# Kernel tuning notes

Measured on AMD Instinct MI355X. Metric: run time of the kernel, lower is better.

Reference implementation:

```python
import jax, jax.numpy as jnp
import numpy as np

N, M, E = 50000, 50000, 1600000
D_IN, HID, OUT = 128, 128, 128


def setup_inputs() -> dict:
    key = jax.random.key(0)
    ks = jax.random.split(key, 8)
    query = jax.random.normal(ks[0], (N, D_IN), jnp.float32)
    memory = jax.random.normal(ks[1], (M, D_IN), jnp.float32)
    adj_vals = jnp.ones((E,), jnp.float32)  # tf.sparse adjacency values (typically 1.0)
    Wq = jax.random.normal(ks[2], (D_IN, HID), jnp.float32) * 0.05
    bq = jnp.zeros((HID,), jnp.float32)
    Wk = jax.random.normal(ks[3], (D_IN, HID), jnp.float32) * 0.05
    bk = jnp.zeros((HID,), jnp.float32)
    Wv = jax.random.normal(ks[4], (D_IN, OUT), jnp.float32) * 0.05
    bv = jnp.zeros((OUT,), jnp.float32)
    rows = jnp.sort(jax.random.randint(ks[5], (E,), 0, N, jnp.int32))
    cols = jax.random.randint(ks[6], (E,), 0, M, jnp.int32)
    return {"query": query, "memory": memory, "adj_vals": adj_vals,
            "Wq": Wq, "bq": bq, "Wk": Wk, "bk": bk, "Wv": Wv, "bv": bv,
            "rows": rows, "cols": cols}


def reference(query, memory, adj_vals, Wq, bq, Wk, bk, Wv, bv, rows, cols):
    n = query.shape[0]
    hid = Wq.shape[1]
    # Dense projections with gelu (tfa.activations.gelu default approximate=True)
    q = jax.nn.gelu(query @ Wq + bq, approximate=True)   # [n, hid]
    k = jax.nn.gelu(memory @ Wk + bk, approximate=True)  # [m, hid]
    v = jax.nn.gelu(memory @ Wv + bv, approximate=True)  # [m, out]
    # Edge-level scores = (q_i . k_j) / sqrt(hid) * adj_val  (== coef * adj_matrix)
    scores = jnp.sum(q[rows] * k[cols], axis=-1)          # [E]
    scores = scores * (adj_vals / jnp.sqrt(jnp.float32(hid)))
    # Sparse softmax over nonzero entries of each row (tf.sparse.softmax)
    row_max = jax.ops.segment_max(scores, rows, num_segments=n, indices_are_sorted=True)
    row_max = jnp.where(jnp.isfinite(row_max), row_max, 0.0)  # rows with no edges
    e = jnp.exp(scores - row_max[rows])
    denom = jax.ops.segment_sum(e, rows, num_segments=n, indices_are_sorted=True)
    w = e / denom[rows]                                   # [E]
    # Sparse-dense matmul: out_i = sum_j w_ij * v_j
    out = jax.ops.segment_sum(w[:, None] * v[cols], rows, num_segments=n, indices_are_sorted=True)
    return out
```

## Files before the change

kernel.cpp:

```cpp
#include <hip/hip_runtime.h>
#include <hip/hip_bf16.h>
#include <math.h>

typedef _Float16 f16x4 __attribute__((ext_vector_type(4)));
typedef _Float16 f16x8 __attribute__((ext_vector_type(8)));
typedef float f32x4 __attribute__((ext_vector_type(4)));

#define DIM 128
#define LDST 136

__global__ __launch_bounds__(256) void prep_w_kernel(
    const float* __restrict__ Wq, const float* __restrict__ Wk,
    const float* __restrict__ Wv, _Float16* __restrict__ Wt)
{
    const float* W = (blockIdx.y == 0) ? Wq : (blockIdx.y == 1) ? Wk : Wv;
    _Float16* dst = Wt + (size_t)blockIdx.y * DIM * DIM;
    int idx = blockIdx.x * 256 + threadIdx.x;
    int k = idx >> 7;
    int n = idx & 127;
    dst[n * DIM + k] = (_Float16)W[idx];
}

__global__ __launch_bounds__(256) void row_ptr_kernel(
    const int* __restrict__ rows, int* __restrict__ row_ptr, int n, int e)
{
    int r = blockIdx.x * 256 + threadIdx.x;
    if (r > n) return;
    if (r == n) { row_ptr[n] = e; return; }
    int lo = 0, hi = e;
    while (lo < hi) {
        int mid = (lo + hi) >> 1;
        if (rows[mid] < r) lo = mid + 1; else hi = mid;
    }
    row_ptr[r] = lo;
}

__global__ __launch_bounds__(256, 2) void proj_gemm_kernel(
    const float* __restrict__ query, const float* __restrict__ memory,
    const _Float16* __restrict__ Wt,
    const float* __restrict__ bq, const float* __restrict__ bk,
    const float* __restrict__ bv,
    _Float16* __restrict__ qf, _Float16* __restrict__ kv, int n, int m)
{
    __shared__ _Float16 xs[128 * LDST];

    int which = blockIdx.y;
    const float* X    = (which == 0) ? query : memory;
    const _Float16* Wm = Wt + (size_t)which * DIM * DIM;
    const float* bias = (which == 0) ? bq : (which == 1) ? bk : bv;
    int R             = (which == 0) ? n : m;
    _Float16* Ybase   = (which == 0) ? qf : (which == 2) ? kv + DIM : kv;
    size_t Ystride    = (which == 0) ? DIM : 2 * DIM;

    int tid = threadIdx.x;
    int rowblock = blockIdx.x * 128;
    if (rowblock >= R) return;

    for (int it = 0; it < 16; ++it) {
        int flat = it * 256 + tid;
        int r  = flat >> 5;
        int c4 = (flat & 31) * 4;
        int gr = rowblock + r;
        if (gr >= R) gr = R - 1;
        float4 x = *(const float4*)(X + (size_t)gr * DIM + c4);
        f16x4 w4;
        w4[0] = (_Float16)x.x; w4[1] = (_Float16)x.y;
        w4[2] = (_Float16)x.z; w4[3] = (_Float16)x.w;
        *(f16x4*)(&xs[r * LDST + c4]) = w4;
    }
    __syncthreads();

    int wave = tid >> 6;
    int lane = tid & 63;
    int quad = lane >> 4;
    int l16  = lane & 15;
    int wrow = wave * 32;

    f16x8 afrag[2][4];
    for (int rt = 0; rt < 2; ++rt)
        for (int ks = 0; ks < 4; ++ks)
            afrag[rt][ks] = *(const f16x8*)(&xs[(wrow + rt * 16 + l16) * LDST + quad * 8 + ks * 32]);

    f32x4 acc[8][2];
    for (int ct = 0; ct < 8; ++ct) { acc[ct][0] = {0,0,0,0}; acc[ct][1] = {0,0,0,0}; }
    for (int ct = 0; ct < 8; ++ct) {
        const _Float16* wp = Wm + (size_t)(ct * 16 + l16) * DIM + quad * 8;
        for (int ks = 0; ks < 4; ++ks) {
            f16x8 b = *(const f16x8*)(wp + ks * 32);
            acc[ct][0] = __builtin_amdgcn_mfma_f32_16x16x32_f16(afrag[0][ks], b, acc[ct][0], 0, 0, 0);
            acc[ct][1] = __builtin_amdgcn_mfma_f32_16x16x32_f16(afrag[1][ks], b, acc[ct][1], 0, 0, 0);
        }
    }

    __syncthreads();
    for (int ct = 0; ct < 8; ++ct) {
        float bval = bias[ct * 16 + l16];
        for (int rt = 0; rt < 2; ++rt) {
            for (int reg = 0; reg < 4; ++reg) {
                float x = acc[ct][rt][reg] + bval;
                float t  = 0.7978845608028654f * (x + 0.044715f * x * x * x);
                float th = 1.0f - 2.0f / (__expf(2.0f * t) + 1.0f);
                float g  = 0.5f * x * (1.0f + th);
                xs[(wrow + rt * 16 + quad * 4 + reg) * LDST + ct * 16 + l16] = (_Float16)g;
            }
        }
    }
    __syncthreads();

    for (int it = 0; it < 8; ++it) {
        int flat = it * 256 + tid;
        int r  = flat >> 4;
        int c8 = (flat & 15) * 8;
        int gr = rowblock + r;
        if (gr < R) {
            f16x8 vv = *(const f16x8*)(&xs[r * LDST + c8]);
            *(f16x8*)(Ybase + (size_t)gr * Ystride + c8) = vv;
        }
    }
}

__global__ __launch_bounds__(256) void edge_attn_kernel(
    const _Float16* __restrict__ qf, const _Float16* __restrict__ kv,
    const float* __restrict__ adj_vals, const int* __restrict__ cols,
    const int* __restrict__ row_ptr, float* __restrict__ out, int n)
{
    int row = blockIdx.x * 4 + (threadIdx.x >> 6);
    if (row >= n) return;
    int lane    = threadIdx.x & 63;
    int quarter = lane >> 4;
    int l16     = lane & 15;

    int start = row_ptr[row];
    int end   = row_ptr[row + 1];

    float qv[8];
    {
        f16x8 qb = *(const f16x8*)(qf + (size_t)row * DIM + l16 * 8);
        for (int j = 0; j < 8; ++j) qv[j] = (float)qb[j];
    }

    float m_q = -1e30f, s_q = 0.0f;
    float acc[8];
    for (int j = 0; j < 8; ++j) acc[j] = 0.0f;

    const float scale = 0.08838834764831845f;

    for (int g = start; g < end; g += 8) {
        int eA = g + quarter;
        int eB = g + 4 + quarter;
        bool vA = eA < end;
        bool vB = eB < end;
        int   cA = vA ? cols[eA]     : 0;
        int   cB = vB ? cols[eB]     : 0;
        float aA = vA ? adj_vals[eA] : 0.0f;
        float aB = vB ? adj_vals[eB] : 0.0f;
        const _Float16* pA = kv + (size_t)cA * 256 + l16 * 8;
        const _Float16* pB = kv + (size_t)cB * 256 + l16 * 8;
        f16x8 kA = *(const f16x8*)pA;
        f16x8 vA8 = *(const f16x8*)(pA + 128);
        f16x8 kB = *(const f16x8*)pB;
        f16x8 vB8 = *(const f16x8*)(pB + 128);

        float dA = 0.0f, dB = 0.0f;
        for (int j = 0; j < 8; ++j) { dA += qv[j] * (float)kA[j]; dB += qv[j] * (float)kB[j]; }
        dA += __shfl_xor(dA, 1); dB += __shfl_xor(dB, 1);
        dA += __shfl_xor(dA, 2); dB += __shfl_xor(dB, 2);
        dA += __shfl_xor(dA, 4); dB += __shfl_xor(dB, 4);
        dA += __shfl_xor(dA, 8); dB += __shfl_xor(dB, 8);

        float sA = vA ? dA * aA * scale : -1e30f;
        float sB = vB ? dB * aB * scale : -1e30f;
        float m_new = fmaxf(m_q, fmaxf(sA, sB));
        float f  = __expf(m_q - m_new);
        float pA_ = vA ? __expf(sA - m_new) : 0.0f;
        float pB_ = vB ? __expf(sB - m_new) : 0.0f;
        s_q = s_q * f + pA_ + pB_;
        m_q = m_new;
        for (int j = 0; j < 8; ++j)
            acc[j] = acc[j] * f + pA_ * (float)vA8[j] + pB_ * (float)vB8[j];
    }

    float m_all = m_q;
    m_all = fmaxf(m_all, __shfl_xor(m_all, 16));
    m_all = fmaxf(m_all, __shfl_xor(m_all, 32));
    float f = __expf(m_q - m_all);
    float s_sc = s_q * f;
    s_sc += __shfl_xor(s_sc, 16);
    s_sc += __shfl_xor(s_sc, 32);
    float inv = (s_sc > 0.0f) ? 1.0f / s_sc : 0.0f;

    float o[8];
    for (int j = 0; j < 8; ++j) {
        float a = acc[j] * f;
        a += __shfl_xor(a, 16);
        a += __shfl_xor(a, 32);
        o[j] = a * inv;
    }
    if (quarter == 0) {
        float4* dst = (float4*)(out + (size_t)row * DIM + l16 * 8);
        dst[0] = make_float4(o[0], o[1], o[2], o[3]);
        dst[1] = make_float4(o[4], o[5], o[6], o[7]);
    }
}

extern "C" void kernel_launch(void* const* d_in, const int* in_sizes, int n_in,
                              void* d_out, int out_size, void* d_ws, size_t ws_size,
                              hipStream_t stream)
{
    const float* query    = (const float*)d_in[0];
    const float* memory   = (const float*)d_in[1];
    const float* adj_vals = (const float*)d_in[2];
    const float* Wq       = (const float*)d_in[3];
    const float* bq       = (const float*)d_in[4];
    const float* Wk       = (const float*)d_in[5];
    const float* bk       = (const float*)d_in[6];
    const float* Wv       = (const float*)d_in[7];
    const float* bv       = (const float*)d_in[8];
    const int*   rows     = (const int*)d_in[9];
    const int*   cols     = (const int*)d_in[10];
    float* out = (float*)d_out;

    int n = in_sizes[0] / DIM;
    int m = in_sizes[1] / DIM;
    int e = in_sizes[9];

    char* ws = (char*)d_ws;
    size_t off = 0;
    _Float16* Wt = (_Float16*)(ws + off); off += (size_t)3 * DIM * DIM * 2;
    _Float16* qf = (_Float16*)(ws + off); off += (size_t)n * DIM * 2;
    _Float16* kv = (_Float16*)(ws + off); off += (size_t)m * 2 * DIM * 2;
    int* row_ptr = (int*)(ws + off);      off += (size_t)(n + 1) * 4;

    prep_w_kernel<<<dim3(64, 3), 256, 0, stream>>>(Wq, Wk, Wv, Wt);

    row_ptr_kernel<<<dim3((n + 1 + 255) / 256), 256, 0, stream>>>(rows, row_ptr, n, e);

    proj_gemm_kernel<<<dim3((n + 127) / 128, 3), 256, 0, stream>>>(
        query, memory, Wt, bq, bk, bv, qf, kv, n, m);

    edge_attn_kernel<<<dim3((n + 3) / 4), 256, 0, stream>>>(
        qf, kv, adj_vals, cols, row_ptr, out, n);
}
```

Baseline: 261.4 us.

## Drop online-softmax max tracking, fuse row search, and use fdot2 in edge kernel

Removes the separate row_ptr kernel; each wave now finds its row's edge range by binary search over the sorted rows, with one lane searching for the start and another for the end. The edge loop maps 8 lanes per edge with 16 elements each and uses packed fp16 dot2 instructions for the q·k dot product. It also drops the running-max rescaling of the online softmax and exponentiates raw scores directly. This cuts per-edge exp and multiply work and a kernel launch, but it risks overflow if scores become large.

Result: slower. 317.2 us (+21.3%).

```diff
diff --git a/kernel.cpp b/kernel.cpp
--- a/kernel.cpp
+++ b/kernel.cpp
@@ -5,6 +5,10 @@
 typedef _Float16 f16x4 __attribute__((ext_vector_type(4)));
 typedef _Float16 f16x8 __attribute__((ext_vector_type(8)));
 typedef float f32x4 __attribute__((ext_vector_type(4)));
+typedef __fp16 hf2 __attribute__((ext_vector_type(2)));
+typedef __fp16 hf8 __attribute__((ext_vector_type(8)));
+
+struct hf2x4 { hf2 a, b, c, d; };
 
 #define DIM 128
 #define LDST 136
@@ -19,20 +23,6 @@
     int k = idx >> 7;
     int n = idx & 127;
     dst[n * DIM + k] = (_Float16)W[idx];
-}
-
-__global__ __launch_bounds__(256) void row_ptr_kernel(
-    const int* __restrict__ rows, int* __restrict__ row_ptr, int n, int e)
-{
-    int r = blockIdx.x * 256 + threadIdx.x;
-    if (r > n) return;
-    if (r == n) { row_ptr[n] = e; return; }
-    int lo = 0, hi = e;
-    while (lo < hi) {
-        int mid = (lo + hi) >> 1;
-        if (rows[mid] < r) lo = mid + 1; else hi = mid;
-    }
-    row_ptr[r] = lo;
 }
 
 __global__ __launch_bounds__(256, 2) void proj_gemm_kernel(
@@ -119,87 +109,113 @@
     }
 }
 
+#if defined(__has_builtin)
+#if __has_builtin(__builtin_amdgcn_fdot2)
+#define HAVE_FDOT2 1
+#endif
+#endif
+
+__device__ __forceinline__ void dot8(float& d, hf8 k8, hf8 q8) {
+#ifdef HAVE_FDOT2
+    hf2x4 K = __builtin_bit_cast(hf2x4, k8);
+    hf2x4 Q = __builtin_bit_cast(hf2x4, q8);
+    d = __builtin_amdgcn_fdot2(K.a, Q.a, d, false);
+    d = __builtin_amdgcn_fdot2(K.b, Q.b, d, false);
+    d = __builtin_amdgcn_fdot2(K.c, Q.c, d, false);
+    d = __builtin_amdgcn_fdot2(K.d, Q.d, d, false);
+#else
+#pragma unroll
+    for (int j = 0; j < 8; ++j) d += (float)k8[j] * (float)q8[j];
+#endif
+}
+
 __global__ __launch_bounds__(256) void edge_attn_kernel(
-    const _Float16* __restrict__ qf, const _Float16* __restrict__ kv,
+    const __fp16* __restrict__ qf, const __fp16* __restrict__ kv,
     const float* __restrict__ adj_vals, const int* __restrict__ cols,
-    const int* __restrict__ row_ptr, float* __restrict__ out, int n)
+    const int* __restrict__ rows, float* __restrict__ out, int n, int e)
 {
     int row = blockIdx.x * 4 + (threadIdx.x >> 6);
     if (row >= n) return;
-    int lane    = threadIdx.x & 63;
-    int quarter = lane >> 4;
-    int l16     = lane & 15;
-
-    int start = row_ptr[row];
-    int end   = row_ptr[row + 1];
-
-    float qv[8];
-    {
-        f16x8 qb = *(const f16x8*)(qf + (size_t)row * DIM + l16 * 8);
-        for (int j = 0; j < 8; ++j) qv[j] = (float)qb[j];
-    }
-
-    float m_q = -1e30f, s_q = 0.0f;
-    float acc[8];
-    for (int j = 0; j < 8; ++j) acc[j] = 0.0f;
+    int lane = threadIdx.x & 63;
+    int g8 = lane >> 3;
+    int l8 = lane & 7;
+
+    int target = row + (lane & 1);
+    int lo = 0, hi = e;
+    while (lo < hi) {
+        int mid = (lo + hi) >> 1;
+        if (rows[mid] < target) lo = mid + 1; else hi = mid;
+    }
+    int start = __shfl(lo, 0);
+    int end   = __shfl(lo, 1);
+
+    const __fp16* qp = qf + (size_t)row * DIM + l8 * 16;
+    hf8 q_lo = *(const hf8*)qp;
+    hf8 q_hi = *(const hf8*)(qp + 8);
+
+    float s_sum = 0.0f;
+    float acc[16];
+#pragma unroll
+    for (int j = 0; j < 16; ++j) acc[j] = 0.0f;
 
     const float scale = 0.08838834764831845f;
 
-    for (int g = start; g < end; g += 8) {
-        int eA = g + quarter;
-        int eB = g + 4 + quarter;
+    for (int base = start; base < end; base += 16) {
+        int eA = base + g8;
+        int eB = base + 8 + g8;
         bool vA = eA < end;
         bool vB = eB < end;
-        int   cA = vA ? cols[eA]     : 0;
-        int   cB = vB ? cols[eB]     : 0;
-        float aA = vA ? adj_vals[eA] : 0.0f;
-        float aB = vB ? adj_vals[eB] : 0.0f;
-        const _Float16* pA = kv + (size_t)cA * 256 + l16 * 8;
-        const _Float16* pB = kv + (size_t)cB * 256 + l16 * 8;
-        f16x8 kA = *(const f16x8*)pA;
-        f16x8 vA8 = *(const f16x8*)(pA + 128);
-        f16x8 kB = *(const f16x8*)pB;
-        f16x8 vB8 = *(const f16x8*)(pB + 128);
+        int last = end - 1;
+        int iA = vA ? eA : last;
+        int iB = vB ? eB : last;
+        int cA = cols[iA];
+        int cB = cols[iB];
+        float aA = adj_vals[iA] * scale;
+        float aB = adj_vals[iB] * scale;
+
+        const __fp16* pA = kv + (size_t)cA * 256 + l8 * 16;
+        const __fp16* pB = kv + (size_t)cB * 256 + l8 * 16;
+        hf8 kA0 = *(const hf8*)pA;
+        hf8 kA1 = *(const hf8*)(pA + 8);
+        hf8 vA0 = *(const hf8*)(pA + 128);
+        hf8 vA1 = *(const hf8*)(pA + 136);
+        hf8 kB0 = *(const hf8*)pB;
+        hf8 kB1 = *(const hf8*)(pB + 8);
+        hf8 vB0 = *(const hf8*)(pB + 128);
+        hf8 vB1 = *(const hf8*)(pB + 136);
 
         float dA = 0.0f, dB = 0.0f;
-        for (int j = 0; j < 8; ++j) { dA += qv[j] * (float)kA[j]; dB += qv[j] * (float)kB[j]; }
+        dot8(dA, kA0, q_lo); dot8(dA, kA1, q_hi);
+        dot8(dB, kB0, q_lo); dot8(dB, kB1, q_hi);
         dA += __shfl_xor(dA, 1); dB += __shfl_xor(dB, 1);
         dA += __shfl_xor(dA, 2); dB += __shfl_xor(dB, 2);
         dA += __shfl_xor(dA, 4); dB += __shfl_xor(dB, 4);
-        dA += __shfl_xor(dA, 8); dB += __shfl_xor(dB, 8);
-
-        float sA = vA ? dA * aA * scale : -1e30f;
-        float sB = vB ? dB * aB * scale : -1e30f;
-        float m_new = fmaxf(m_q, fmaxf(sA, sB));
-        float f  = __expf(m_q - m_new);
-        float pA_ = vA ? __expf(sA - m_new) : 0.0f;
-        float pB_ = vB ? __expf(sB - m_new) : 0.0f;
-        s_q = s_q * f + pA_ + pB_;
-        m_q = m_new;
-        for (int j = 0; j < 8; ++j)
-            acc[j] = acc[j] * f + pA_ * (float)vA8[j] + pB_ * (float)vB8[j];
-    }
-
-    float m_all = m_q;
-    m_all = fmaxf(m_all, __shfl_xor(m_all, 16));
-    m_all = fmaxf(m_all, __shfl_xor(m_all, 32));
-    float f = __expf(m_q - m_all);
-    float s_sc = s_q * f;
-    s_sc += __shfl_xor(s_sc, 16);
-    s_sc += __shfl_xor(s_sc, 32);
-    float inv = (s_sc > 0.0f) ? 1.0f / s_sc : 0.0f;
-
-    float o[8];
-    for (int j = 0; j < 8; ++j) {
-        float a = acc[j] * f;
-        a += __shfl_xor(a, 16);
-        a += __shfl_xor(a, 32);
-        o[j] = a * inv;
-    }
-    if (quarter == 0) {
-        float4* dst = (float4*)(out + (size_t)row * DIM + l16 * 8);
-        dst[0] = make_float4(o[0], o[1], o[2], o[3]);
-        dst[1] = make_float4(o[4], o[5], o[6], o[7]);
+
+        float pA_ = vA ? __expf(dA * aA) : 0.0f;
+        float pB_ = vB ? __expf(dB * aB) : 0.0f;
+        s_sum += pA_ + pB_;
+#pragma unroll
+        for (int j = 0; j < 8; ++j) acc[j]     += pA_ * (float)vA0[j] + pB_ * (float)vB0[j];
+#pragma unroll
+        for (int j = 0; j < 8; ++j) acc[j + 8] += pA_ * (float)vA1[j] + pB_ * (float)vB1[j];
+    }
+
+#pragma unroll
+    for (int mask = 8; mask <= 32; mask <<= 1) {
+        s_sum += __shfl_xor(s_sum, mask);
+#pragma unroll
+        for (int j = 0; j < 16; ++j) acc[j] += __shfl_xor(acc[j], mask);
+    }
+    float inv = (s_sum > 0.0f) ? 1.0f / s_sum : 0.0f;
+
+    if (g8 == 0) {
+        float* dst = out + (size_t)row * DIM + l8 * 16;
+#pragma unroll
+        for (int c = 0; c < 4; ++c) {
+            float4 o = make_float4(acc[c*4+0] * inv, acc[c*4+1] * inv,
+                                   acc[c*4+2] * inv, acc[c*4+3] * inv);
+            *(float4*)(dst + c * 4) = o;
+        }
     }
 }
 
@@ -229,15 +245,12 @@
     _Float16* Wt = (_Float16*)(ws + off); off += (size_t)3 * DIM * DIM * 2;
     _Float16* qf = (_Float16*)(ws + off); off += (size_t)n * DIM * 2;
     _Float16* kv = (_Float16*)(ws + off); off += (size_t)m * 2 * DIM * 2;
-    int* row_ptr = (int*)(ws + off);      off += (size_t)(n + 1) * 4;
 
     prep_w_kernel<<<dim3(64, 3), 256, 0, stream>>>(Wq, Wk, Wv, Wt);
-
-    row_ptr_kernel<<<dim3((n + 1 + 255) / 256), 256, 0, stream>>>(rows, row_ptr, n, e);
 
     proj_gemm_kernel<<<dim3((n + 127) / 128, 3), 256, 0, stream>>>(
         query, memory, Wt, bq, bk, bv, qf, kv, n, m);
 
     edge_attn_kernel<<<dim3((n + 3) / 4), 256, 0, stream>>>(
-        qf, kv, adj_vals, cols, row_ptr, out, n);
-}
+        (const __fp16*)qf, (const __fp16*)kv, adj_vals, cols, rows, out, n, e);
+}
```
